# Optimization experiments

Hardware: AMD Instinct MI355X
Metric: run time of the kernel (lower is better)

## Reference

```python
import jax, jax.numpy as jnp
import numpy as np

TEMPERATURE = 0.07
EPS = 1e-8  # torch CosineSimilarity eps


def setup_inputs() -> dict:
    key = jax.random.key(0)
    k1, k2, k3 = jax.random.split(key, 3)
    N, D = 8192, 512
    features = jax.random.normal(k1, (N, D), dtype=jnp.float32)
    positive_mask = jax.random.randint(k2, (N, N), 0, 2, dtype=jnp.int32)
    negative_mask = jax.random.randint(k3, (N, N), 0, 2, dtype=jnp.int32)
    return {"features": features, "positive_mask": positive_mask, "negative_mask": negative_mask}


def reference(features, positive_mask, negative_mask):
    N = positive_mask.shape[0]
    self_contrast = 1.0 - jnp.eye(N, dtype=features.dtype)  # zero diagonal
    pos = positive_mask.astype(features.dtype) * self_contrast  # [N, N]
    neg = negative_mask.astype(features.dtype) * self_contrast  # [N, N]

    # cosine similarity via normalized matmul (same math as broadcasted CosineSimilarity)
    norm = jnp.maximum(jnp.linalg.norm(features, axis=1, keepdims=True), EPS)
    fn = features / norm  # [N, D]
    sim = jnp.matmul(fn, fn.T) / TEMPERATURE  # [N, N]

    logits_max = jax.lax.stop_gradient(jnp.max(sim, axis=1, keepdims=True))
    e = jnp.exp(sim - logits_max)  # [N, N]

    positives = e * pos
    log_neg_sum = jnp.log(jnp.sum(e * neg, axis=1, keepdims=True))  # [N, 1]
    log_prob = positives - log_neg_sum  # [N, N] (faithful to source: exp-masked, not log)

    cardinal = jnp.sum(pos, axis=1)
    cardinal = jnp.where(cardinal == 0, 1.0, cardinal)
    log_prob_sum = jnp.sum(log_prob * pos, axis=1)
    loss = -log_prob_sum / cardinal
    return jnp.mean(loss)
```

## Files before the change

kernel.cpp:

```cpp
#include <hip/hip_runtime.h>
#include <hip/hip_bf16.h>
#include <math.h>

#define NN 8192
#define DD 512
#define INV_T 14.285714285714286f

typedef __attribute__((ext_vector_type(8))) short s16x8;
typedef __attribute__((ext_vector_type(4))) float f32x4;

__device__ __forceinline__ unsigned short f32_to_bf16(float f) {
  unsigned int u = __float_as_uint(f);
  u += 0x7FFFu + ((u >> 16) & 1u);
  return (unsigned short)(u >> 16);
}

__device__ __forceinline__ void async16(const void* g, void* l) {
  __builtin_amdgcn_global_load_lds((__attribute__((address_space(1))) void*)(void*)g,
                                   (__attribute__((address_space(3))) void*)l,
                                   16, 0, 0);
}

__global__ __launch_bounds__(256) void normalize_kernel(const float* __restrict__ f,
                                                        unsigned short* __restrict__ fnb) {
  const int wave = threadIdx.x >> 6;
  const int lane = threadIdx.x & 63;
  const int row  = blockIdx.x * 4 + wave;
  const float* src = f + (size_t)row * DD + lane * 8;
  float4 v0 = *(const float4*)src;
  float4 v1 = *(const float4*)(src + 4);
  float ss = v0.x*v0.x + v0.y*v0.y + v0.z*v0.z + v0.w*v0.w
           + v1.x*v1.x + v1.y*v1.y + v1.z*v1.z + v1.w*v1.w;
  #pragma unroll
  for (int o = 32; o; o >>= 1) ss += __shfl_xor(ss, o);
  const float r = 1.0f / fmaxf(sqrtf(ss), 1e-8f);
  ushort4 a, b;
  a.x = f32_to_bf16(v0.x * r); a.y = f32_to_bf16(v0.y * r);
  a.z = f32_to_bf16(v0.z * r); a.w = f32_to_bf16(v0.w * r);
  b.x = f32_to_bf16(v1.x * r); b.y = f32_to_bf16(v1.y * r);
  b.z = f32_to_bf16(v1.z * r); b.w = f32_to_bf16(v1.w * r);
  unsigned short* dst = fnb + (size_t)row * DD + lane * 8;
  *(ushort4*)dst = a;
  *(ushort4*)(dst + 4) = b;
}

__global__ __launch_bounds__(256) void fused_kernel(const unsigned short* __restrict__ fnb,
                                                    const int* __restrict__ posm,
                                                    const int* __restrict__ negm,
                                                    float* __restrict__ Spos,
                                                    float* __restrict__ Sneg,
                                                    float* __restrict__ Pcnt) {
  const int bi = blockIdx.y;
  const int bj = blockIdx.x;
  if (bj < bi) return;
  const int I = bi * 128;
  const int J = bj * 128;

  const int tid  = threadIdx.x;
  const int wave = tid >> 6;
  const int lane = tid & 63;
  const int wm = wave >> 1;
  const int wn = wave & 1;
  const int q   = lane >> 4;
  const int c16 = lane & 15;

  __shared__ alignas(16) unsigned short lA[128 * 32];
  __shared__ alignas(16) unsigned short lB[128 * 32];

  f32x4 acc[4][4];
  const f32x4 z4 = {0.f, 0.f, 0.f, 0.f};
  #pragma unroll
  for (int mt = 0; mt < 4; ++mt)
    #pragma unroll
    for (int nt = 0; nt < 4; ++nt) acc[mt][nt] = z4;

  for (int kk = 0; kk < DD / 32; ++kk) {
    const int k0 = kk * 32;
    #pragma unroll
    for (int c = 0; c < 2; ++c) {
      const int fidx = tid + c * 256;
      const int row  = fidx >> 2;
      const int ke   = (fidx & 3) * 8;
      async16(fnb + (size_t)(I + row) * DD + k0 + ke, (char*)lA + fidx * 16);
      async16(fnb + (size_t)(J + row) * DD + k0 + ke, (char*)lB + fidx * 16);
    }
    __syncthreads();

    s16x8 aF[4], bF[4];
    #pragma unroll
    for (int t = 0; t < 4; ++t) {
      const int arow = wm * 64 + t * 16 + c16;
      aF[t] = *(const s16x8*)((const char*)lA + arow * 64 + q * 16);
      const int brow = wn * 64 + t * 16 + c16;
      bF[t] = *(const s16x8*)((const char*)lB + brow * 64 + q * 16);
    }
    #pragma unroll
    for (int mt = 0; mt < 4; ++mt)
      #pragma unroll
      for (int nt = 0; nt < 4; ++nt)
        acc[mt][nt] = __builtin_amdgcn_mfma_f32_16x16x32_bf16(aF[mt], bF[nt], acc[mt][nt], 0, 0, 0);
    __syncthreads();
  }

  float tsp[4] = {0,0,0,0}, tsn[4] = {0,0,0,0}, tpc[4] = {0,0,0,0};
  const bool offdiag = (bi != bj);

  #pragma unroll
  for (int mt = 0; mt < 4; ++mt) {
    float dsp[4] = {0,0,0,0}, dsn[4] = {0,0,0,0}, dpc[4] = {0,0,0,0};
    const int rbase = I + wm * 64 + mt * 16 + q * 4;
    #pragma unroll
    for (int nt = 0; nt < 4; ++nt) {
      const int col = J + wn * 64 + nt * 16 + c16;
      float e[4];
      #pragma unroll
      for (int r = 0; r < 4; ++r)
        e[r] = __expf(acc[mt][nt][r] * INV_T - INV_T);
      #pragma unroll
      for (int r = 0; r < 4; ++r) {
        const int row = rbase + r;
        const int off = row * NN + col;
        float pf = (float)posm[off];
        float nf = (float)negm[off];
        if (row == col) { pf = 0.f; nf = 0.f; }
        dsp[r] = fmaf(e[r], pf, dsp[r]);
        dsn[r] = fmaf(e[r], nf, dsn[r]);
        dpc[r] += pf;
      }
      if (offdiag) {
        const int toff = col * NN + rbase;
        const int4 pT = *(const int4*)(posm + toff);
        const int4 nT = *(const int4*)(negm + toff);
        tsp[nt] += e[0]*(float)pT.x + e[1]*(float)pT.y + e[2]*(float)pT.z + e[3]*(float)pT.w;
        tsn[nt] += e[0]*(float)nT.x + e[1]*(float)nT.y + e[2]*(float)nT.z + e[3]*(float)nT.w;
        tpc[nt] += (float)(pT.x + pT.y + pT.z + pT.w);
      }
    }
    #pragma unroll
    for (int r = 0; r < 4; ++r) {
      float a = dsp[r], b = dsn[r], p = dpc[r];
      #pragma unroll
      for (int o = 1; o <= 8; o <<= 1) {
        a += __shfl_xor(a, o);
        b += __shfl_xor(b, o);
        p += __shfl_xor(p, o);
      }
      if (c16 == 0) {
        atomicAdd(&Spos[rbase + r], a);
        atomicAdd(&Sneg[rbase + r], b);
        atomicAdd(&Pcnt[rbase + r], p);
      }
    }
  }

  if (offdiag) {
    #pragma unroll
    for (int nt = 0; nt < 4; ++nt) {
      float a = tsp[nt], b = tsn[nt], p = tpc[nt];
      a += __shfl_xor(a, 16); a += __shfl_xor(a, 32);
      b += __shfl_xor(b, 16); b += __shfl_xor(b, 32);
      p += __shfl_xor(p, 16); p += __shfl_xor(p, 32);
      if (q == 0) {
        const int col = J + wn * 64 + nt * 16 + c16;
        atomicAdd(&Spos[col], a);
        atomicAdd(&Sneg[col], b);
        atomicAdd(&Pcnt[col], p);
      }
    }
  }
}

__global__ __launch_bounds__(256) void finalize_kernel(const float* __restrict__ Spos,
                                                       const float* __restrict__ Sneg,
                                                       const float* __restrict__ Pcnt,
                                                       float* __restrict__ out) {
  float local = 0.f;
  for (int i = threadIdx.x; i < NN; i += 256) {
    const float sp = Spos[i], sn = Sneg[i], pc = Pcnt[i];
    const float card = (pc == 0.f) ? 1.f : pc;
    local += (logf(sn) * pc - sp) / card;
  }
  #pragma unroll
  for (int o = 32; o; o >>= 1) local += __shfl_xor(local, o);
  __shared__ float red[4];
  if ((threadIdx.x & 63) == 0) red[threadIdx.x >> 6] = local;
  __syncthreads();
  if (threadIdx.x == 0)
    out[0] = (red[0] + red[1] + red[2] + red[3]) * (1.0f / (float)NN);
}

extern "C" void kernel_launch(void* const* d_in, const int* in_sizes, int n_in,
                              void* d_out, int out_size, void* d_ws, size_t ws_size,
                              hipStream_t stream) {
  const float* feat = (const float*)d_in[0];
  const int* posm   = (const int*)d_in[1];
  const int* negm   = (const int*)d_in[2];
  float* out = (float*)d_out;

  unsigned short* fnb = (unsigned short*)d_ws;
  float* Spos = (float*)((char*)d_ws + (size_t)NN * DD * 2);
  float* Sneg = Spos + NN;
  float* Pcnt = Sneg + NN;

  hipMemsetAsync(Spos, 0, 3 * NN * sizeof(float), stream);
  normalize_kernel<<<NN / 4, 256, 0, stream>>>(feat, fnb);
  dim3 grid(64, 64);
  fused_kernel<<<grid, 256, 0, stream>>>(fnb, posm, negm, Spos, Sneg, Pcnt);
  finalize_kernel<<<1, 256, 0, stream>>>(Spos, Sneg, Pcnt, out);
}
```

Measured before the change: 655.6 us.

## Pack masks into bitsets, use triangular grid, and swizzle LDS tiles

A new pack kernel streams both int32 masks once with nontemporal loads and compresses them into 64-bit ballot bitsets. The fused kernel then reads bit words instead of scattered int32 values, including the transposed accesses, and gets positive counts from popcount. The grid launches only the upper-triangle blocks through an index decode, and the LDS tile layout is XOR-swizzled to reduce bank conflicts. The cost is an extra full pass over the masks plus 16 MB of bitset writes, in exchange for much less scattered mask traffic inside the GEMM epilogue.

```diff
diff --git a/kernel.cpp b/kernel.cpp
--- a/kernel.cpp
+++ b/kernel.cpp
@@ -5,6 +5,7 @@
 #define NN 8192
 #define DD 512
 #define INV_T 14.285714285714286f
+#define NWPR 128
 
 typedef __attribute__((ext_vector_type(8))) short s16x8;
 typedef __attribute__((ext_vector_type(4))) float f32x4;
@@ -44,15 +45,47 @@
   *(ushort4*)(dst + 4) = b;
 }
 
+__global__ __launch_bounds__(256) void pack_kernel(const int* __restrict__ posm,
+                                                   const int* __restrict__ negm,
+                                                   unsigned long long* __restrict__ pb,
+                                                   unsigned long long* __restrict__ nb) {
+  const int lane = threadIdx.x & 63;
+  const long long gw = (long long)((blockIdx.x * 256 + threadIdx.x) >> 6);
+  const long long nwaves = (long long)((gridDim.x * 256) >> 6);
+  const long long NW = (long long)NN * NN / 64;
+  for (long long w0 = gw * 8; w0 < NW; w0 += nwaves * 8) {
+    unsigned long long bp[8], bn[8];
+    #pragma unroll
+    for (int u = 0; u < 8; ++u) {
+      const size_t idx = (size_t)(w0 + u) * 64 + lane;
+      const int p = __builtin_nontemporal_load(posm + idx);
+      const int n = __builtin_nontemporal_load(negm + idx);
+      bp[u] = __ballot(p != 0);
+      bn[u] = __ballot(n != 0);
+    }
+    if (lane == 0) {
+      #pragma unroll
+      for (int u = 0; u < 8; u += 2) {
+        ulonglong2 vp; vp.x = bp[u]; vp.y = bp[u + 1];
+        ulonglong2 vn; vn.x = bn[u]; vn.y = bn[u + 1];
+        *(ulonglong2*)(pb + w0 + u) = vp;
+        *(ulonglong2*)(nb + w0 + u) = vn;
+      }
+    }
+  }
+}
+
 __global__ __launch_bounds__(256) void fused_kernel(const unsigned short* __restrict__ fnb,
-                                                    const int* __restrict__ posm,
-                                                    const int* __restrict__ negm,
+                                                    const unsigned long long* __restrict__ pb,
+                                                    const unsigned long long* __restrict__ nb,
                                                     float* __restrict__ Spos,
                                                     float* __restrict__ Sneg,
                                                     float* __restrict__ Pcnt) {
-  const int bi = blockIdx.y;
-  const int bj = blockIdx.x;
-  if (bj < bi) return;
+  const int bid = blockIdx.x;
+  int bi = (int)(64.5 - sqrt(64.5 * 64.5 - 2.0 * (double)bid));
+  while (64 * bi - bi * (bi - 1) / 2 > bid) --bi;
+  while (64 * (bi + 1) - (bi + 1) * bi / 2 <= bid) ++bi;
+  const int bj = bi + (bid - (64 * bi - bi * (bi - 1) / 2));
   const int I = bi * 128;
   const int J = bj * 128;
 
@@ -80,9 +113,10 @@
     for (int c = 0; c < 2; ++c) {
       const int fidx = tid + c * 256;
       const int row  = fidx >> 2;
-      const int ke   = (fidx & 3) * 8;
-      async16(fnb + (size_t)(I + row) * DD + k0 + ke, (char*)lA + fidx * 16);
-      async16(fnb + (size_t)(J + row) * DD + k0 + ke, (char*)lB + fidx * 16);
+      const int p    = fidx & 3;
+      const int csrc = (p ^ ((row >> 1) & 3)) & 3;
+      async16(fnb + (size_t)(I + row) * DD + k0 + csrc * 8, (char*)lA + fidx * 16);
+      async16(fnb + (size_t)(J + row) * DD + k0 + csrc * 8, (char*)lB + fidx * 16);
     }
     __syncthreads();
 
@@ -90,9 +124,11 @@
     #pragma unroll
     for (int t = 0; t < 4; ++t) {
       const int arow = wm * 64 + t * 16 + c16;
-      aF[t] = *(const s16x8*)((const char*)lA + arow * 64 + q * 16);
+      const int apos = (q ^ ((arow >> 1) & 3)) & 3;
+      aF[t] = *(const s16x8*)((const char*)lA + arow * 64 + apos * 16);
       const int brow = wn * 64 + t * 16 + c16;
-      bF[t] = *(const s16x8*)((const char*)lB + brow * 64 + q * 16);
+      const int bpos = (q ^ ((brow >> 1) & 3)) & 3;
+      bF[t] = *(const s16x8*)((const char*)lB + brow * 64 + bpos * 16);
     }
     #pragma unroll
     for (int mt = 0; mt < 4; ++mt)
@@ -102,53 +138,73 @@
     __syncthreads();
   }
 
-  float tsp[4] = {0,0,0,0}, tsn[4] = {0,0,0,0}, tpc[4] = {0,0,0,0};
   const bool offdiag = (bi != bj);
-
-  #pragma unroll
-  for (int mt = 0; mt < 4; ++mt) {
-    float dsp[4] = {0,0,0,0}, dsn[4] = {0,0,0,0}, dpc[4] = {0,0,0,0};
-    const int rbase = I + wm * 64 + mt * 16 + q * 4;
+  const bool hasdiag = (bi == bj) && (wm == wn);
+  const int jw = bj * 2 + wn;
+
+  unsigned long long pT[4], nT[4];
+  if (offdiag) {
     #pragma unroll
     for (int nt = 0; nt < 4; ++nt) {
       const int col = J + wn * 64 + nt * 16 + c16;
+      const size_t tw = (size_t)col * NWPR + bi * 2 + wm;
+      pT[nt] = pb[tw];
+      nT[nt] = nb[tw];
+    }
+  }
+  float tsp[4] = {0,0,0,0}, tsn[4] = {0,0,0,0};
+
+  #pragma unroll
+  for (int mt = 0; mt < 4; ++mt) {
+    const int rbase = I + wm * 64 + mt * 16 + q * 4;
+    unsigned long long pw[4], nw[4];
+    #pragma unroll
+    for (int r = 0; r < 4; ++r) {
+      const size_t w = (size_t)(rbase + r) * NWPR + jw;
+      pw[r] = pb[w];
+      nw[r] = nb[w];
+      if (hasdiag) {
+        const unsigned long long m = ~(1ULL << (mt * 16 + q * 4 + r));
+        pw[r] &= m;
+        nw[r] &= m;
+      }
+    }
+    float dsp[4] = {0,0,0,0}, dsn[4] = {0,0,0,0};
+    #pragma unroll
+    for (int nt = 0; nt < 4; ++nt) {
       float e[4];
       #pragma unroll
       for (int r = 0; r < 4; ++r)
         e[r] = __expf(acc[mt][nt][r] * INV_T - INV_T);
+      const int bpos = nt * 16 + c16;
       #pragma unroll
       for (int r = 0; r < 4; ++r) {
-        const int row = rbase + r;
-        const int off = row * NN + col;
-        float pf = (float)posm[off];
-        float nf = (float)negm[off];
-        if (row == col) { pf = 0.f; nf = 0.f; }
+        const float pf = (float)((pw[r] >> bpos) & 1ULL);
+        const float nf = (float)((nw[r] >> bpos) & 1ULL);
         dsp[r] = fmaf(e[r], pf, dsp[r]);
         dsn[r] = fmaf(e[r], nf, dsn[r]);
-        dpc[r] += pf;
       }
       if (offdiag) {
-        const int toff = col * NN + rbase;
-        const int4 pT = *(const int4*)(posm + toff);
-        const int4 nT = *(const int4*)(negm + toff);
-        tsp[nt] += e[0]*(float)pT.x + e[1]*(float)pT.y + e[2]*(float)pT.z + e[3]*(float)pT.w;
-        tsn[nt] += e[0]*(float)nT.x + e[1]*(float)nT.y + e[2]*(float)nT.z + e[3]*(float)nT.w;
-        tpc[nt] += (float)(pT.x + pT.y + pT.z + pT.w);
+        const int bt = mt * 16 + q * 4;
+        #pragma unroll
+        for (int r = 0; r < 4; ++r) {
+          tsp[nt] = fmaf(e[r], (float)((pT[nt] >> (bt + r)) & 1ULL), tsp[nt]);
+          tsn[nt] = fmaf(e[r], (float)((nT[nt] >> (bt + r)) & 1ULL), tsn[nt]);
+        }
       }
     }
     #pragma unroll
     for (int r = 0; r < 4; ++r) {
-      float a = dsp[r], b = dsn[r], p = dpc[r];
+      float a = dsp[r], b = dsn[r];
       #pragma unroll
       for (int o = 1; o <= 8; o <<= 1) {
         a += __shfl_xor(a, o);
         b += __shfl_xor(b, o);
-        p += __shfl_xor(p, o);
       }
       if (c16 == 0) {
         atomicAdd(&Spos[rbase + r], a);
         atomicAdd(&Sneg[rbase + r], b);
-        atomicAdd(&Pcnt[rbase + r], p);
+        atomicAdd(&Pcnt[rbase + r], (float)__popcll(pw[r]));
       }
     }
   }
@@ -156,15 +212,14 @@
   if (offdiag) {
     #pragma unroll
     for (int nt = 0; nt < 4; ++nt) {
-      float a = tsp[nt], b = tsn[nt], p = tpc[nt];
+      float a = tsp[nt], b = tsn[nt];
       a += __shfl_xor(a, 16); a += __shfl_xor(a, 32);
       b += __shfl_xor(b, 16); b += __shfl_xor(b, 32);
-      p += __shfl_xor(p, 16); p += __shfl_xor(p, 32);
       if (q == 0) {
         const int col = J + wn * 64 + nt * 16 + c16;
         atomicAdd(&Spos[col], a);
         atomicAdd(&Sneg[col], b);
-        atomicAdd(&Pcnt[col], p);
+        atomicAdd(&Pcnt[col], (float)__popcll(pT[nt]));
       }
     }
   }
@@ -197,14 +252,17 @@
   const int* negm   = (const int*)d_in[2];
   float* out = (float*)d_out;
 
-  unsigned short* fnb = (unsigned short*)d_ws;
-  float* Spos = (float*)((char*)d_ws + (size_t)NN * DD * 2);
+  char* ws = (char*)d_ws;
+  unsigned short* fnb = (unsigned short*)ws;
+  unsigned long long* pbit = (unsigned long long*)(ws + (size_t)8 * 1024 * 1024);
+  unsigned long long* nbit = (unsigned long long*)(ws + (size_t)16 * 1024 * 1024);
+  float* Spos = (float*)(ws + (size_t)24 * 1024 * 1024);
   float* Sneg = Spos + NN;
   float* Pcnt = Sneg + NN;
 
   hipMemsetAsync(Spos, 0, 3 * NN * sizeof(float), stream);
   normalize_kernel<<<NN / 4, 256, 0, stream>>>(feat, fnb);
-  dim3 grid(64, 64);
-  fused_kernel<<<grid, 256, 0, stream>>>(fnb, posm, negm, Spos, Sneg, Pcnt);
+  pack_kernel<<<4096, 256, 0, stream>>>(posm, negm, pbit, nbit);
+  fused_kernel<<<2080, 256, 0, stream>>>(fnb, pbit, nbit, Spos, Sneg, Pcnt);
   finalize_kernel<<<1, 256, 0, stream>>>(Spos, Sneg, Pcnt, out);
 }
```

Measured after the change: 669.6 us. +2.1%, slower.
